# Optimization experiments

Hardware: AMD Instinct MI355X
Metric: run time of the kernel (lower is better)

## Reference

```python
import jax, jax.numpy as jnp
import numpy as np

N = 100000   # nodes
E = 1600000  # edges (avg degree 16)
D = 32       # feature / hidden dim


def setup_inputs() -> dict:
    key = jax.random.key(0)
    k_x, k_e, kq, kk, kv, ko = jax.random.split(key, 6)
    s = 1.0 / np.sqrt(D).astype(np.float32)
    x = jax.random.normal(k_x, (N, D), dtype=jnp.float32)
    edge_index = jax.random.randint(k_e, (2, E), 0, N, dtype=jnp.int64)
    Wq = jax.random.normal(kq, (D, D), dtype=jnp.float32) * s
    Wk = jax.random.normal(kk, (D, D), dtype=jnp.float32) * s
    Wv = jax.random.normal(kv, (D, D), dtype=jnp.float32) * s
    Wo = jax.random.normal(ko, (D, D), dtype=jnp.float32) * s
    return {"x": x, "edge_index": edge_index, "Wq": Wq, "Wk": Wk, "Wv": Wv, "Wo": Wo}


def reference(x, edge_index, Wq, Wk, Wv, Wo):
    sender, receiver = edge_index[0], edge_index[1]
    n = x.shape[0]
    scale = x.shape[1] ** -0.5  # hidden_dim == D
    Q = x @ Wq  # [N, D]
    K = x @ Wk
    V = x @ Wv
    # per-edge attention scores
    scores = jnp.sum(Q[receiver] * K[sender], axis=1) * scale  # [E]
    # numerically-stable segment softmax over incoming edges of each receiver
    smax = jax.ops.segment_max(scores, receiver, num_segments=n)  # [N]
    alpha = jnp.exp(scores - smax[receiver])  # [E]
    Z = jax.ops.segment_sum(alpha, receiver, num_segments=n)  # [N]
    alpha = alpha / (Z[receiver] + 1e-6)
    # weighted aggregation of sender values
    out = jax.ops.segment_sum(alpha[:, None] * V[sender], receiver, num_segments=n)  # [N, D]
    return x + out @ Wo
```

## Files before the change

kernel.cpp:

```cpp
#include <hip/hip_runtime.h>
#include <hip/hip_bf16.h>

#define DIM 32
#define RPB 32
#define RCR 512
#define NCMAX 256
#define CAPC 9216
#define PBLK 256

__device__ __forceinline__ float b2f(ushort h) {
    union { float f; unsigned u; } u; u.u = ((unsigned)h) << 16; return u.f;
}
__device__ __forceinline__ float h2f(ushort u) {
    _Float16 h; __builtin_memcpy(&h, &u, 2); return (float)h;
}
__device__ __forceinline__ ushort f2h(float f) {
    _Float16 h = (_Float16)f; ushort u; __builtin_memcpy(&u, &h, 2); return u;
}

__device__ __forceinline__ int load_idx(const int* __restrict__ idx, size_t pos,
                                        int mode, int n) {
    int v = mode ? idx[2 * pos] : idx[pos];
    return v < 0 ? 0 : (v >= n ? n - 1 : v);
}
__device__ __forceinline__ float load_f(const void* p, size_t i, int bf) {
    return bf ? b2f(((const ushort*)p)[i]) : ((const float*)p)[i];
}

__global__ void __launch_bounds__(256)
qkv_kernel(const void* __restrict__ x_, const void* __restrict__ Wq_,
           const void* __restrict__ Wk_, const void* __restrict__ Wv_,
           int N, int nc, ushort* __restrict__ Q, ushort* __restrict__ KV,
           unsigned* __restrict__ gcur) {
    __shared__ float sW[3][DIM * DIM];
    __shared__ float sx[8][DIM];
    __shared__ int sBf;

    const int tid = threadIdx.x;
    if (tid < 64) {
        int e = (((const ushort*)x_)[2 * tid] >> 7) & 0xFF;
        unsigned long long bb = __ballot(e >= 100 && e <= 135);
        if (tid == 0) sBf = (__popcll(bb) >= 56);
    }
    if (blockIdx.x == 0) {
        for (int i = tid; i < nc; i += 256) gcur[i] = (unsigned)i * CAPC;
    }
    __syncthreads();
    const int bf = sBf;

    for (int i = tid; i < DIM * DIM; i += 256) {
        sW[0][i] = load_f(Wq_, i, bf);
        sW[1][i] = load_f(Wk_, i, bf);
        sW[2][i] = load_f(Wv_, i, bf);
    }
    const int lr  = tid >> 5;
    const int d   = tid & 31;
    const int row = blockIdx.x * 8 + lr;
    if (row < N) sx[lr][d] = load_f(x_, (size_t)row * DIM + d, bf);
    __syncthreads();
    if (row >= N) return;

    float aq = 0.f, ak = 0.f, av = 0.f;
#pragma unroll
    for (int k = 0; k < DIM; ++k) {
        const float xk = sx[lr][k];
        aq += xk * sW[0][k * DIM + d];
        ak += xk * sW[1][k * DIM + d];
        av += xk * sW[2][k * DIM + d];
    }
    Q[(size_t)row * DIM + d]      = f2h(aq * 0.17677669529663687f);
    KV[(size_t)row * 64 + d]      = f2h(ak);
    KV[(size_t)row * 64 + 32 + d] = f2h(av);
}

__global__ void __launch_bounds__(256)
place_kernel(const int* __restrict__ idx, int E, int N, int nc,
             unsigned* __restrict__ gcur, unsigned* __restrict__ bedges) {
    __shared__ int h[NCMAX];
    __shared__ int goff[NCMAX];
    __shared__ int sMode;

    const int tid = threadIdx.x;
    if (tid < 64) {
        unsigned long long mm = __ballot(idx[2 * tid + 1] != 0);
        if (tid == 0) sMode = (mm == 0ULL);
    }
    for (int i = tid; i < nc; i += 256) h[i] = 0;
    __syncthreads();
    const int mode = sMode;

    const int per = (E + gridDim.x - 1) / gridDim.x;
    const int e0 = blockIdx.x * per;
    const int e1 = min(e0 + per, E);

    for (int e = e0 + tid; e < e1; e += 256) {
        const int r = load_idx(idx, (size_t)E + e, mode, N);
        atomicAdd(&h[r >> 9], 1);
    }
    __syncthreads();
    for (int i = tid; i < nc; i += 256) {
        const int v = h[i];
        goff[i] = v ? (int)atomicAdd(&gcur[i], (unsigned)v) : 0;
        h[i] = 0;
    }
    __syncthreads();
    for (int e = e0 + tid; e < e1; e += 256) {
        const int r = load_idx(idx, (size_t)E + e, mode, N);
        const int s = load_idx(idx, (size_t)e, mode, N);
        const int cb = r >> 9;
        const int p = goff[cb] + atomicAdd(&h[cb], 1);
        if (p < (cb + 1) * CAPC)
            bedges[p] = (unsigned)s | ((unsigned)(r & (RCR - 1)) << 17);
    }
}

__global__ void __launch_bounds__(1024)
rsort_kernel(unsigned* __restrict__ bedges, const unsigned* __restrict__ gcur,
             int* __restrict__ rbase, int* __restrict__ rcount) {
    __shared__ unsigned eL[CAPC];
    __shared__ int cnt[RCR];
    __shared__ int wsum[8];

    const int tid = threadIdx.x;
    const int c = blockIdx.x;
    const unsigned s0 = (unsigned)c * CAPC;
    int m = (int)(gcur[c] - s0);
    if (m < 0) m = 0; if (m > CAPC) m = CAPC;

    if (tid < RCR) cnt[tid] = 0;
    __syncthreads();
    for (int i = tid; i < m; i += 1024) {
        const unsigned e = bedges[s0 + i];
        eL[i] = e;
        atomicAdd(&cnt[(e >> 17) & (RCR - 1)], 1);
    }
    __syncthreads();

    const int lane = tid & 63, w = tid >> 6;
    const int v = (tid < RCR) ? cnt[tid] : 0;
    int x = v;
#pragma unroll
    for (int o = 1; o < 64; o <<= 1) { int t = __shfl_up(x, o); if (lane >= o) x += t; }
    if (tid < RCR && lane == 63) wsum[w] = x;
    __syncthreads();
    if (tid == 0) {
        int a = 0;
#pragma unroll
        for (int k = 0; k < 8; ++k) { int t = wsum[k]; wsum[k] = a; a += t; }
    }
    __syncthreads();
    int excl = 0;
    if (tid < RCR) {
        excl = x - v + wsum[w];
        rbase[c * RCR + tid]  = (int)s0 + excl;
        rcount[c * RCR + tid] = v;
    }
    __syncthreads();
    if (tid < RCR) cnt[tid] = (int)s0 + excl;
    __syncthreads();
    for (int i = tid; i < m; i += 1024) {
        const unsigned e = eL[i];
        const int p = atomicAdd(&cnt[(e >> 17) & (RCR - 1)], 1);
        bedges[p] = e & 0x1FFFF;
    }
}

__global__ void __launch_bounds__(256)
agg_kernel(const ushort* __restrict__ Q, const ushort* __restrict__ KV,
           const unsigned* __restrict__ bedges, const int* __restrict__ rbase,
           const int* __restrict__ rcount, const void* __restrict__ x_,
           const void* __restrict__ Wo_, int N, float* __restrict__ out) {
    __shared__ float sWo[DIM * DIM];
    __shared__ float accS[RPB][DIM + 1];
    __shared__ float Zs[RPB];
    __shared__ unsigned sQ[RPB * 16];
    __shared__ int sBf;

    const int tid = threadIdx.x;
    if (tid < 64) {
        int e = (((const ushort*)x_)[2 * tid] >> 7) & 0xFF;
        unsigned long long bb = __ballot(e >= 100 && e <= 135);
        if (tid == 0) sBf = (__popcll(bb) >= 56);
    }
    const int r0 = blockIdx.x * RPB;
    const int nr = min(RPB, N - r0);
    __syncthreads();
    const int bf = sBf;

    for (int i = tid; i < DIM * DIM; i += 256) sWo[i] = load_f(Wo_, i, bf);
    for (int i = tid; i < nr * 16; i += 256)
        sQ[i] = ((const unsigned*)(Q + (size_t)r0 * DIM))[i];
    __syncthreads();

    const int w    = tid >> 6;
    const int lane = tid & 63;
    const int i8   = lane >> 3;
    const int j    = lane & 7;

    for (int rl = w; rl < nr; rl += 4) {
        const int r   = r0 + rl;
        const int deg = rcount[r];
        const int o0  = rbase[r];
        const ushort4 qh = *(const ushort4*)((const ushort*)sQ + rl * DIM + j * 4);
        const float q0 = h2f(qh.x), q1 = h2f(qh.y), q2 = h2f(qh.z), q3 = h2f(qh.w);

        float ax = 0.f, ay = 0.f, az = 0.f, aw = 0.f, zs = 0.f;
        const int chunks = (deg + 7) >> 3;
        const int dm1 = deg - 1;

        int cc = 0;
        for (; cc + 2 <= chunks; cc += 2) {
            const int c0 = cc * 8 + i8;
            const int c1 = c0 + 8;
            const bool ok0 = (c0 < deg);
            const bool ok1 = (c1 < deg);
            const int s0 = (int)bedges[o0 + (ok0 ? c0 : dm1)];
            const int s1 = (int)bedges[o0 + (ok1 ? c1 : dm1)];
            const ushort* kvA = KV + (size_t)s0 * 64;
            const ushort* kvB = KV + (size_t)s1 * 64;

            const ushort4 khA = *(const ushort4*)(kvA + j * 4);
            const ushort4 vhA = *(const ushort4*)(kvA + 32 + j * 4);
            const ushort4 khB = *(const ushort4*)(kvB + j * 4);
            const ushort4 vhB = *(const ushort4*)(kvB + 32 + j * 4);

            float pA = h2f(khA.x) * q0;
            float pB = h2f(khB.x) * q0;
            pA = fmaf(h2f(khA.y), q1, pA);  pB = fmaf(h2f(khB.y), q1, pB);
            pA = fmaf(h2f(khA.z), q2, pA);  pB = fmaf(h2f(khB.z), q2, pB);
            pA = fmaf(h2f(khA.w), q3, pA);  pB = fmaf(h2f(khB.w), q3, pB);

            pA += __shfl_xor(pA, 1);        pB += __shfl_xor(pB, 1);
            pA += __shfl_xor(pA, 2);        pB += __shfl_xor(pB, 2);
            pA += __shfl_xor(pA, 4);        pB += __shfl_xor(pB, 4);

            pA = fminf(fmaxf(pA, -60.f), 60.f);
            pB = fminf(fmaxf(pB, -60.f), 60.f);
            const float aA = ok0 ? __expf(pA) : 0.f;
            const float aB = ok1 ? __expf(pB) : 0.f;

            ax = fmaf(h2f(vhA.x), aA, ax);  ax = fmaf(h2f(vhB.x), aB, ax);
            ay = fmaf(h2f(vhA.y), aA, ay);  ay = fmaf(h2f(vhB.y), aB, ay);
            az = fmaf(h2f(vhA.z), aA, az);  az = fmaf(h2f(vhB.z), aB, az);
            aw = fmaf(h2f(vhA.w), aA, aw);  aw = fmaf(h2f(vhB.w), aB, aw);
            zs += aA + aB;
        }
        if (cc < chunks) {
            const int c = cc * 8 + i8;
            const bool ok = (c < deg);
            const int s = (int)bedges[o0 + (ok ? c : dm1)];
            const ushort* kv = KV + (size_t)s * 64;
            const ushort4 kh = *(const ushort4*)(kv + j * 4);
            const ushort4 vh = *(const ushort4*)(kv + 32 + j * 4);

            float p = h2f(kh.x) * q0;
            p = fmaf(h2f(kh.y), q1, p);
            p = fmaf(h2f(kh.z), q2, p);
            p = fmaf(h2f(kh.w), q3, p);
            p += __shfl_xor(p, 1);
            p += __shfl_xor(p, 2);
            p += __shfl_xor(p, 4);
            p = fminf(fmaxf(p, -60.f), 60.f);
            const float a = ok ? __expf(p) : 0.f;

            ax = fmaf(h2f(vh.x), a, ax);
            ay = fmaf(h2f(vh.y), a, ay);
            az = fmaf(h2f(vh.z), a, az);
            aw = fmaf(h2f(vh.w), a, aw);
            zs += a;
        }
#pragma unroll
        for (int o = 8; o < 64; o <<= 1) {
            ax += __shfl_xor(ax, o); ay += __shfl_xor(ay, o);
            az += __shfl_xor(az, o); aw += __shfl_xor(aw, o);
            zs += __shfl_xor(zs, o);
        }
        if (i8 == 0) {
            float* ar = accS[rl];
            ar[j * 4 + 0] = ax; ar[j * 4 + 1] = ay;
            ar[j * 4 + 2] = az; ar[j * 4 + 3] = aw;
            if (j == 0) Zs[rl] = zs;
        }
    }
    __syncthreads();

    const int lr = tid >> 5;
    const int d  = tid & 31;
#pragma unroll
    for (int it = 0; it < RPB / 8; ++it) {
        const int rl = it * 8 + lr;
        if (rl < nr) {
            const float inv = 1.f / (Zs[rl] + 1e-6f);
            float o = 0.f;
#pragma unroll
            for (int k = 0; k < DIM; ++k) o += accS[rl][k] * sWo[k * DIM + d];
            const size_t oi = (size_t)(r0 + rl) * DIM + d;
            out[oi] = load_f(x_, oi, bf) + inv * o;
        }
    }
}

extern "C" void kernel_launch(void* const* d_in, const int* in_sizes, int n_in,
                              void* d_out, int out_size, void* d_ws, size_t ws_size,
                              hipStream_t stream) {
    const void* x   = d_in[0];
    const int*  idx = (const int*)d_in[1];
    const void* Wq  = d_in[2];
    const void* Wk  = d_in[3];
    const void* Wv  = d_in[4];
    const void* Wo  = d_in[5];
    float* out = (float*)d_out;

    const int N = in_sizes[0] / DIM;
    const int E = in_sizes[1] / 2;
    const int nc = (N + RCR - 1) / RCR;
    const size_t N32 = (size_t)N * DIM;

    ushort*   Q      = (ushort*)d_ws;
    ushort*   KV     = Q + N32;
    unsigned* bedges = (unsigned*)(KV + (size_t)N * 64);
    unsigned* gcur   = bedges + (size_t)nc * CAPC;
    int*      rbase  = (int*)(gcur + NCMAX);
    int*      rcount = rbase + (size_t)nc * RCR;

    qkv_kernel<<<(N + 7) / 8, 256, 0, stream>>>(x, Wq, Wk, Wv, N, nc, Q, KV, gcur);
    place_kernel<<<PBLK, 256, 0, stream>>>(idx, E, N, nc, gcur, bedges);
    rsort_kernel<<<nc, 1024, 0, stream>>>(bedges, gcur, rbase, rcount);
    agg_kernel<<<(N + RPB - 1) / RPB, 256, 0, stream>>>(Q, KV, bedges, rbase,
                                                        rcount, x, Wo, N, out);
}
```

Baseline: 212.3 us.

## Fuse four kernels into one cooperative persistent kernel with grid syncs

Merges the QKV projection, edge bucket placement, per-chunk receiver sort and attention aggregation into a single cooperative kernel with 256 blocks of 1024 threads. Phases are separated by grid.sync(), and shared memory is reused across phases through a union. The aim is to remove the launch gaps between kernels. In exchange, occupancy drops to one large block per CU with a fixed grid, the aggregation phase loses the fine-grained scheduling of many small blocks, and each phase waits on grid-wide barriers.

```diff
diff --git a/kernel.cpp b/kernel.cpp
--- a/kernel.cpp
+++ b/kernel.cpp
@@ -1,12 +1,15 @@
 #include <hip/hip_runtime.h>
 #include <hip/hip_bf16.h>
+#include <hip/hip_cooperative_groups.h>
+
+namespace cg = cooperative_groups;
 
 #define DIM 32
-#define RPB 32
 #define RCR 512
 #define NCMAX 256
 #define CAPC 9216
-#define PBLK 256
+#define GRID 256
+#define BLK 1024
 
 __device__ __forceinline__ float b2f(ushort h) {
     union { float f; unsigned u; } u; u.u = ((unsigned)h) << 16; return u.f;
@@ -17,7 +20,6 @@
 __device__ __forceinline__ ushort f2h(float f) {
     _Float16 h = (_Float16)f; ushort u; __builtin_memcpy(&u, &h, 2); return u;
 }
-
 __device__ __forceinline__ int load_idx(const int* __restrict__ idx, size_t pos,
                                         int mode, int n) {
     int v = mode ? idx[2 * pos] : idx[pos];
@@ -27,275 +29,264 @@
     return bf ? b2f(((const ushort*)p)[i]) : ((const float*)p)[i];
 }
 
-__global__ void __launch_bounds__(256)
-qkv_kernel(const void* __restrict__ x_, const void* __restrict__ Wq_,
-           const void* __restrict__ Wk_, const void* __restrict__ Wv_,
-           int N, int nc, ushort* __restrict__ Q, ushort* __restrict__ KV,
-           unsigned* __restrict__ gcur) {
-    __shared__ float sW[3][DIM * DIM];
-    __shared__ float sx[8][DIM];
-    __shared__ int sBf;
+union SMem {
+    struct { float sW[3][DIM * DIM]; float sx[32][DIM]; } qkv;
+    struct { int h[NCMAX]; int goff[NCMAX]; } place;
+    struct { unsigned eL[CAPC]; int cnt[RCR]; int wsum[16]; } sort;
+    struct { float sWo[DIM * DIM]; unsigned sQ[128 * 16];
+             float accS[128][DIM + 1]; float Zs[128]; } agg;
+};
+
+__global__ void __launch_bounds__(BLK)
+mega_kernel(const void* __restrict__ x_, const int* __restrict__ idx,
+            const void* __restrict__ Wq_, const void* __restrict__ Wk_,
+            const void* __restrict__ Wv_, const void* __restrict__ Wo_,
+            int N, int E, int nc,
+            ushort* __restrict__ Q, ushort* __restrict__ KV,
+            unsigned* __restrict__ bedges, unsigned* __restrict__ gcur,
+            int* __restrict__ rbase, int* __restrict__ rcount,
+            float* __restrict__ out) {
+    cg::grid_group grid = cg::this_grid();
+    __shared__ SMem sm;
+    __shared__ int sBf, sMode;
 
     const int tid = threadIdx.x;
+
     if (tid < 64) {
         int e = (((const ushort*)x_)[2 * tid] >> 7) & 0xFF;
         unsigned long long bb = __ballot(e >= 100 && e <= 135);
-        if (tid == 0) sBf = (__popcll(bb) >= 56);
+        unsigned long long mm = __ballot(idx[2 * tid + 1] != 0);
+        if (tid == 0) { sBf = (__popcll(bb) >= 56); sMode = (mm == 0ULL); }
     }
     if (blockIdx.x == 0) {
-        for (int i = tid; i < nc; i += 256) gcur[i] = (unsigned)i * CAPC;
+        for (int i = tid; i < nc; i += BLK) gcur[i] = (unsigned)i * CAPC;
     }
     __syncthreads();
-    const int bf = sBf;
-
-    for (int i = tid; i < DIM * DIM; i += 256) {
-        sW[0][i] = load_f(Wq_, i, bf);
-        sW[1][i] = load_f(Wk_, i, bf);
-        sW[2][i] = load_f(Wv_, i, bf);
-    }
-    const int lr  = tid >> 5;
-    const int d   = tid & 31;
-    const int row = blockIdx.x * 8 + lr;
-    if (row < N) sx[lr][d] = load_f(x_, (size_t)row * DIM + d, bf);
-    __syncthreads();
-    if (row >= N) return;
-
-    float aq = 0.f, ak = 0.f, av = 0.f;
-#pragma unroll
-    for (int k = 0; k < DIM; ++k) {
-        const float xk = sx[lr][k];
-        aq += xk * sW[0][k * DIM + d];
-        ak += xk * sW[1][k * DIM + d];
-        av += xk * sW[2][k * DIM + d];
-    }
-    Q[(size_t)row * DIM + d]      = f2h(aq * 0.17677669529663687f);
-    KV[(size_t)row * 64 + d]      = f2h(ak);
-    KV[(size_t)row * 64 + 32 + d] = f2h(av);
-}
-
-__global__ void __launch_bounds__(256)
-place_kernel(const int* __restrict__ idx, int E, int N, int nc,
-             unsigned* __restrict__ gcur, unsigned* __restrict__ bedges) {
-    __shared__ int h[NCMAX];
-    __shared__ int goff[NCMAX];
-    __shared__ int sMode;
-
-    const int tid = threadIdx.x;
-    if (tid < 64) {
-        unsigned long long mm = __ballot(idx[2 * tid + 1] != 0);
-        if (tid == 0) sMode = (mm == 0ULL);
-    }
-    for (int i = tid; i < nc; i += 256) h[i] = 0;
-    __syncthreads();
-    const int mode = sMode;
-
-    const int per = (E + gridDim.x - 1) / gridDim.x;
-    const int e0 = blockIdx.x * per;
-    const int e1 = min(e0 + per, E);
-
-    for (int e = e0 + tid; e < e1; e += 256) {
-        const int r = load_idx(idx, (size_t)E + e, mode, N);
-        atomicAdd(&h[r >> 9], 1);
-    }
-    __syncthreads();
-    for (int i = tid; i < nc; i += 256) {
-        const int v = h[i];
-        goff[i] = v ? (int)atomicAdd(&gcur[i], (unsigned)v) : 0;
-        h[i] = 0;
-    }
-    __syncthreads();
-    for (int e = e0 + tid; e < e1; e += 256) {
-        const int r = load_idx(idx, (size_t)E + e, mode, N);
-        const int s = load_idx(idx, (size_t)e, mode, N);
-        const int cb = r >> 9;
-        const int p = goff[cb] + atomicAdd(&h[cb], 1);
-        if (p < (cb + 1) * CAPC)
-            bedges[p] = (unsigned)s | ((unsigned)(r & (RCR - 1)) << 17);
-    }
-}
-
-__global__ void __launch_bounds__(1024)
-rsort_kernel(unsigned* __restrict__ bedges, const unsigned* __restrict__ gcur,
-             int* __restrict__ rbase, int* __restrict__ rcount) {
-    __shared__ unsigned eL[CAPC];
-    __shared__ int cnt[RCR];
-    __shared__ int wsum[8];
-
-    const int tid = threadIdx.x;
-    const int c = blockIdx.x;
-    const unsigned s0 = (unsigned)c * CAPC;
-    int m = (int)(gcur[c] - s0);
-    if (m < 0) m = 0; if (m > CAPC) m = CAPC;
-
-    if (tid < RCR) cnt[tid] = 0;
-    __syncthreads();
-    for (int i = tid; i < m; i += 1024) {
-        const unsigned e = bedges[s0 + i];
-        eL[i] = e;
-        atomicAdd(&cnt[(e >> 17) & (RCR - 1)], 1);
-    }
-    __syncthreads();
-
-    const int lane = tid & 63, w = tid >> 6;
-    const int v = (tid < RCR) ? cnt[tid] : 0;
-    int x = v;
-#pragma unroll
-    for (int o = 1; o < 64; o <<= 1) { int t = __shfl_up(x, o); if (lane >= o) x += t; }
-    if (tid < RCR && lane == 63) wsum[w] = x;
-    __syncthreads();
-    if (tid == 0) {
-        int a = 0;
-#pragma unroll
-        for (int k = 0; k < 8; ++k) { int t = wsum[k]; wsum[k] = a; a += t; }
-    }
-    __syncthreads();
-    int excl = 0;
-    if (tid < RCR) {
-        excl = x - v + wsum[w];
-        rbase[c * RCR + tid]  = (int)s0 + excl;
-        rcount[c * RCR + tid] = v;
-    }
-    __syncthreads();
-    if (tid < RCR) cnt[tid] = (int)s0 + excl;
-    __syncthreads();
-    for (int i = tid; i < m; i += 1024) {
-        const unsigned e = eL[i];
-        const int p = atomicAdd(&cnt[(e >> 17) & (RCR - 1)], 1);
-        bedges[p] = e & 0x1FFFF;
-    }
-}
-
-__global__ void __launch_bounds__(256)
-agg_kernel(const ushort* __restrict__ Q, const ushort* __restrict__ KV,
-           const unsigned* __restrict__ bedges, const int* __restrict__ rbase,
-           const int* __restrict__ rcount, const void* __restrict__ x_,
-           const void* __restrict__ Wo_, int N, float* __restrict__ out) {
-    __shared__ float sWo[DIM * DIM];
-    __shared__ float accS[RPB][DIM + 1];
-    __shared__ float Zs[RPB];
-    __shared__ unsigned sQ[RPB * 16];
-    __shared__ int sBf;
-
-    const int tid = threadIdx.x;
-    if (tid < 64) {
-        int e = (((const ushort*)x_)[2 * tid] >> 7) & 0xFF;
-        unsigned long long bb = __ballot(e >= 100 && e <= 135);
-        if (tid == 0) sBf = (__popcll(bb) >= 56);
-    }
-    const int r0 = blockIdx.x * RPB;
-    const int nr = min(RPB, N - r0);
-    __syncthreads();
-    const int bf = sBf;
-
-    for (int i = tid; i < DIM * DIM; i += 256) sWo[i] = load_f(Wo_, i, bf);
-    for (int i = tid; i < nr * 16; i += 256)
-        sQ[i] = ((const unsigned*)(Q + (size_t)r0 * DIM))[i];
-    __syncthreads();
-
-    const int w    = tid >> 6;
-    const int lane = tid & 63;
-    const int i8   = lane >> 3;
-    const int j    = lane & 7;
-
-    for (int rl = w; rl < nr; rl += 4) {
-        const int r   = r0 + rl;
-        const int deg = rcount[r];
-        const int o0  = rbase[r];
-        const ushort4 qh = *(const ushort4*)((const ushort*)sQ + rl * DIM + j * 4);
-        const float q0 = h2f(qh.x), q1 = h2f(qh.y), q2 = h2f(qh.z), q3 = h2f(qh.w);
-
-        float ax = 0.f, ay = 0.f, az = 0.f, aw = 0.f, zs = 0.f;
-        const int chunks = (deg + 7) >> 3;
-        const int dm1 = deg - 1;
-
-        int cc = 0;
-        for (; cc + 2 <= chunks; cc += 2) {
-            const int c0 = cc * 8 + i8;
-            const int c1 = c0 + 8;
-            const bool ok0 = (c0 < deg);
-            const bool ok1 = (c1 < deg);
-            const int s0 = (int)bedges[o0 + (ok0 ? c0 : dm1)];
-            const int s1 = (int)bedges[o0 + (ok1 ? c1 : dm1)];
-            const ushort* kvA = KV + (size_t)s0 * 64;
-            const ushort* kvB = KV + (size_t)s1 * 64;
-
-            const ushort4 khA = *(const ushort4*)(kvA + j * 4);
-            const ushort4 vhA = *(const ushort4*)(kvA + 32 + j * 4);
-            const ushort4 khB = *(const ushort4*)(kvB + j * 4);
-            const ushort4 vhB = *(const ushort4*)(kvB + 32 + j * 4);
-
-            float pA = h2f(khA.x) * q0;
-            float pB = h2f(khB.x) * q0;
-            pA = fmaf(h2f(khA.y), q1, pA);  pB = fmaf(h2f(khB.y), q1, pB);
-            pA = fmaf(h2f(khA.z), q2, pA);  pB = fmaf(h2f(khB.z), q2, pB);
-            pA = fmaf(h2f(khA.w), q3, pA);  pB = fmaf(h2f(khB.w), q3, pB);
-
-            pA += __shfl_xor(pA, 1);        pB += __shfl_xor(pB, 1);
-            pA += __shfl_xor(pA, 2);        pB += __shfl_xor(pB, 2);
-            pA += __shfl_xor(pA, 4);        pB += __shfl_xor(pB, 4);
-
-            pA = fminf(fmaxf(pA, -60.f), 60.f);
-            pB = fminf(fmaxf(pB, -60.f), 60.f);
-            const float aA = ok0 ? __expf(pA) : 0.f;
-            const float aB = ok1 ? __expf(pB) : 0.f;
-
-            ax = fmaf(h2f(vhA.x), aA, ax);  ax = fmaf(h2f(vhB.x), aB, ax);
-            ay = fmaf(h2f(vhA.y), aA, ay);  ay = fmaf(h2f(vhB.y), aB, ay);
-            az = fmaf(h2f(vhA.z), aA, az);  az = fmaf(h2f(vhB.z), aB, az);
-            aw = fmaf(h2f(vhA.w), aA, aw);  aw = fmaf(h2f(vhB.w), aB, aw);
-            zs += aA + aB;
-        }
-        if (cc < chunks) {
-            const int c = cc * 8 + i8;
-            const bool ok = (c < deg);
-            const int s = (int)bedges[o0 + (ok ? c : dm1)];
-            const ushort* kv = KV + (size_t)s * 64;
-            const ushort4 kh = *(const ushort4*)(kv + j * 4);
-            const ushort4 vh = *(const ushort4*)(kv + 32 + j * 4);
-
-            float p = h2f(kh.x) * q0;
-            p = fmaf(h2f(kh.y), q1, p);
-            p = fmaf(h2f(kh.z), q2, p);
-            p = fmaf(h2f(kh.w), q3, p);
-            p += __shfl_xor(p, 1);
-            p += __shfl_xor(p, 2);
-            p += __shfl_xor(p, 4);
-            p = fminf(fmaxf(p, -60.f), 60.f);
-            const float a = ok ? __expf(p) : 0.f;
-
-            ax = fmaf(h2f(vh.x), a, ax);
-            ay = fmaf(h2f(vh.y), a, ay);
-            az = fmaf(h2f(vh.z), a, az);
-            aw = fmaf(h2f(vh.w), a, aw);
-            zs += a;
-        }
-#pragma unroll
-        for (int o = 8; o < 64; o <<= 1) {
-            ax += __shfl_xor(ax, o); ay += __shfl_xor(ay, o);
-            az += __shfl_xor(az, o); aw += __shfl_xor(aw, o);
-            zs += __shfl_xor(zs, o);
-        }
-        if (i8 == 0) {
-            float* ar = accS[rl];
-            ar[j * 4 + 0] = ax; ar[j * 4 + 1] = ay;
-            ar[j * 4 + 2] = az; ar[j * 4 + 3] = aw;
-            if (j == 0) Zs[rl] = zs;
-        }
-    }
-    __syncthreads();
-
-    const int lr = tid >> 5;
-    const int d  = tid & 31;
-#pragma unroll
-    for (int it = 0; it < RPB / 8; ++it) {
-        const int rl = it * 8 + lr;
-        if (rl < nr) {
-            const float inv = 1.f / (Zs[rl] + 1e-6f);
-            float o = 0.f;
-#pragma unroll
-            for (int k = 0; k < DIM; ++k) o += accS[rl][k] * sWo[k * DIM + d];
-            const size_t oi = (size_t)(r0 + rl) * DIM + d;
-            out[oi] = load_f(x_, oi, bf) + inv * o;
+    const int bf = sBf, mode = sMode;
+
+    for (int i = tid; i < DIM * DIM; i += BLK) {
+        sm.qkv.sW[0][i] = load_f(Wq_, i, bf);
+        sm.qkv.sW[1][i] = load_f(Wk_, i, bf);
+        sm.qkv.sW[2][i] = load_f(Wv_, i, bf);
+    }
+    {
+        const int lr = tid >> 5;
+        const int d  = tid & 31;
+        for (int base = blockIdx.x * 32; base < N; base += GRID * 32) {
+            const int row = base + lr;
+            __syncthreads();
+            if (row < N) sm.qkv.sx[lr][d] = load_f(x_, (size_t)row * DIM + d, bf);
+            __syncthreads();
+            if (row < N) {
+                float aq = 0.f, ak = 0.f, av = 0.f;
+#pragma unroll
+                for (int k = 0; k < DIM; ++k) {
+                    const float xk = sm.qkv.sx[lr][k];
+                    aq += xk * sm.qkv.sW[0][k * DIM + d];
+                    ak += xk * sm.qkv.sW[1][k * DIM + d];
+                    av += xk * sm.qkv.sW[2][k * DIM + d];
+                }
+                Q[(size_t)row * DIM + d]      = f2h(aq * 0.17677669529663687f);
+                KV[(size_t)row * 64 + d]      = f2h(ak);
+                KV[(size_t)row * 64 + 32 + d] = f2h(av);
+            }
+        }
+    }
+    grid.sync();
+
+    {
+        const int per = (E + GRID - 1) / GRID;
+        const int e0 = blockIdx.x * per;
+        const int e1 = min(e0 + per, E);
+        for (int i = tid; i < nc; i += BLK) sm.place.h[i] = 0;
+        __syncthreads();
+        for (int e = e0 + tid; e < e1; e += BLK) {
+            const int r = load_idx(idx, (size_t)E + e, mode, N);
+            atomicAdd(&sm.place.h[r >> 9], 1);
+        }
+        __syncthreads();
+        for (int i = tid; i < nc; i += BLK) {
+            const int v = sm.place.h[i];
+            sm.place.goff[i] = v ? (int)atomicAdd(&gcur[i], (unsigned)v) : 0;
+            sm.place.h[i] = 0;
+        }
+        __syncthreads();
+        for (int e = e0 + tid; e < e1; e += BLK) {
+            const int r = load_idx(idx, (size_t)E + e, mode, N);
+            const int s = load_idx(idx, (size_t)e, mode, N);
+            const int cb = r >> 9;
+            const int p = sm.place.goff[cb] + atomicAdd(&sm.place.h[cb], 1);
+            if (p < (cb + 1) * CAPC)
+                bedges[p] = (unsigned)s | ((unsigned)(r & (RCR - 1)) << 17);
+        }
+    }
+    grid.sync();
+
+    for (int c = blockIdx.x; c < nc; c += GRID) {
+        const unsigned s0 = (unsigned)c * CAPC;
+        int m = (int)(gcur[c] - s0);
+        if (m < 0) m = 0; if (m > CAPC) m = CAPC;
+
+        if (tid < RCR) sm.sort.cnt[tid] = 0;
+        __syncthreads();
+        for (int i = tid; i < m; i += BLK) {
+            const unsigned e = bedges[s0 + i];
+            sm.sort.eL[i] = e;
+            atomicAdd(&sm.sort.cnt[(e >> 17) & (RCR - 1)], 1);
+        }
+        __syncthreads();
+
+        const int lane = tid & 63, w = tid >> 6;
+        const int v = (tid < RCR) ? sm.sort.cnt[tid] : 0;
+        int x = v;
+#pragma unroll
+        for (int o = 1; o < 64; o <<= 1) {
+            int t = __shfl_up(x, o); if (lane >= o) x += t;
+        }
+        if (tid < RCR && lane == 63) sm.sort.wsum[w] = x;
+        __syncthreads();
+        if (tid == 0) {
+            int a = 0;
+#pragma unroll
+            for (int k = 0; k < 8; ++k) { int t = sm.sort.wsum[k]; sm.sort.wsum[k] = a; a += t; }
+        }
+        __syncthreads();
+        int excl = 0;
+        if (tid < RCR) {
+            excl = x - v + sm.sort.wsum[w];
+            rbase[c * RCR + tid]  = (int)s0 + excl;
+            rcount[c * RCR + tid] = v;
+        }
+        __syncthreads();
+        if (tid < RCR) sm.sort.cnt[tid] = (int)s0 + excl;
+        __syncthreads();
+        for (int i = tid; i < m; i += BLK) {
+            const unsigned e = sm.sort.eL[i];
+            const int p = atomicAdd(&sm.sort.cnt[(e >> 17) & (RCR - 1)], 1);
+            bedges[p] = e & 0x1FFFF;
+        }
+        __syncthreads();
+    }
+    grid.sync();
+
+    for (int i = tid; i < DIM * DIM; i += BLK) sm.agg.sWo[i] = load_f(Wo_, i, bf);
+    {
+        const int ngrp = (N + 127) >> 7;
+        const int w    = tid >> 6;
+        const int lane = tid & 63;
+        const int i8   = lane >> 3;
+        const int j    = lane & 7;
+        const int lr   = tid >> 5;
+        const int d    = tid & 31;
+
+        for (int g = blockIdx.x; g < ngrp; g += GRID) {
+            const int r0 = g << 7;
+            const int nr = min(128, N - r0);
+            __syncthreads();
+            for (int i = tid; i < nr * 16; i += BLK)
+                sm.agg.sQ[i] = ((const unsigned*)(Q + (size_t)r0 * DIM))[i];
+            __syncthreads();
+
+            for (int rl = w; rl < nr; rl += 16) {
+                const int r   = r0 + rl;
+                const int deg = rcount[r];
+                const int o0  = rbase[r];
+                const ushort4 qh = *(const ushort4*)((const ushort*)sm.agg.sQ + rl * DIM + j * 4);
+                const float q0 = h2f(qh.x), q1 = h2f(qh.y), q2 = h2f(qh.z), q3 = h2f(qh.w);
+
+                float ax = 0.f, ay = 0.f, az = 0.f, aw = 0.f, zs = 0.f;
+                const int chunks = (deg + 7) >> 3;
+                const int dm1 = deg - 1;
+
+                int cc = 0;
+                for (; cc + 2 <= chunks; cc += 2) {
+                    const int c0 = cc * 8 + i8;
+                    const int c1 = c0 + 8;
+                    const bool ok0 = (c0 < deg);
+                    const bool ok1 = (c1 < deg);
+                    const int sA = (int)bedges[o0 + (ok0 ? c0 : dm1)];
+                    const int sB = (int)bedges[o0 + (ok1 ? c1 : dm1)];
+                    const ushort* kvA = KV + (size_t)sA * 64;
+                    const ushort* kvB = KV + (size_t)sB * 64;
+
+                    const ushort4 khA = *(const ushort4*)(kvA + j * 4);
+                    const ushort4 vhA = *(const ushort4*)(kvA + 32 + j * 4);
+                    const ushort4 khB = *(const ushort4*)(kvB + j * 4);
+                    const ushort4 vhB = *(const ushort4*)(kvB + 32 + j * 4);
+
+                    float pA = h2f(khA.x) * q0;
+                    float pB = h2f(khB.x) * q0;
+                    pA = fmaf(h2f(khA.y), q1, pA);  pB = fmaf(h2f(khB.y), q1, pB);
+                    pA = fmaf(h2f(khA.z), q2, pA);  pB = fmaf(h2f(khB.z), q2, pB);
+                    pA = fmaf(h2f(khA.w), q3, pA);  pB = fmaf(h2f(khB.w), q3, pB);
+
+                    pA += __shfl_xor(pA, 1);        pB += __shfl_xor(pB, 1);
+                    pA += __shfl_xor(pA, 2);        pB += __shfl_xor(pB, 2);
+                    pA += __shfl_xor(pA, 4);        pB += __shfl_xor(pB, 4);
+
+                    pA = fminf(fmaxf(pA, -60.f), 60.f);
+                    pB = fminf(fmaxf(pB, -60.f), 60.f);
+                    const float aA = ok0 ? __expf(pA) : 0.f;
+                    const float aB = ok1 ? __expf(pB) : 0.f;
+
+                    ax = fmaf(h2f(vhA.x), aA, ax);  ax = fmaf(h2f(vhB.x), aB, ax);
+                    ay = fmaf(h2f(vhA.y), aA, ay);  ay = fmaf(h2f(vhB.y), aB, ay);
+                    az = fmaf(h2f(vhA.z), aA, az);  az = fmaf(h2f(vhB.z), aB, az);
+                    aw = fmaf(h2f(vhA.w), aA, aw);  aw = fmaf(h2f(vhB.w), aB, aw);
+                    zs += aA + aB;
+                }
+                if (cc < chunks) {
+                    const int c = cc * 8 + i8;
+                    const bool ok = (c < deg);
+                    const int s = (int)bedges[o0 + (ok ? c : dm1)];
+                    const ushort* kv = KV + (size_t)s * 64;
+                    const ushort4 kh = *(const ushort4*)(kv + j * 4);
+                    const ushort4 vh = *(const ushort4*)(kv + 32 + j * 4);
+
+                    float p = h2f(kh.x) * q0;
+                    p = fmaf(h2f(kh.y), q1, p);
+                    p = fmaf(h2f(kh.z), q2, p);
+                    p = fmaf(h2f(kh.w), q3, p);
+                    p += __shfl_xor(p, 1);
+                    p += __shfl_xor(p, 2);
+                    p += __shfl_xor(p, 4);
+                    p = fminf(fmaxf(p, -60.f), 60.f);
+                    const float a = ok ? __expf(p) : 0.f;
+
+                    ax = fmaf(h2f(vh.x), a, ax);
+                    ay = fmaf(h2f(vh.y), a, ay);
+                    az = fmaf(h2f(vh.z), a, az);
+                    aw = fmaf(h2f(vh.w), a, aw);
+                    zs += a;
+                }
+#pragma unroll
+                for (int o = 8; o < 64; o <<= 1) {
+                    ax += __shfl_xor(ax, o); ay += __shfl_xor(ay, o);
+                    az += __shfl_xor(az, o); aw += __shfl_xor(aw, o);
+                    zs += __shfl_xor(zs, o);
+                }
+                if (i8 == 0) {
+                    float* ar = sm.agg.accS[rl];
+                    ar[j * 4 + 0] = ax; ar[j * 4 + 1] = ay;
+                    ar[j * 4 + 2] = az; ar[j * 4 + 3] = aw;
+                    if (j == 0) sm.agg.Zs[rl] = zs;
+                }
+            }
+            __syncthreads();
+
+#pragma unroll
+            for (int it = 0; it < 4; ++it) {
+                const int rl = it * 32 + lr;
+                if (rl < nr) {
+                    const float inv = 1.f / (sm.agg.Zs[rl] + 1e-6f);
+                    float o = 0.f;
+#pragma unroll
+                    for (int k = 0; k < DIM; ++k)
+                        o += sm.agg.accS[rl][k] * sm.agg.sWo[k * DIM + d];
+                    const size_t oi = (size_t)(r0 + rl) * DIM + d;
+                    out[oi] = load_f(x_, oi, bf) + inv * o;
+                }
+            }
         }
     }
 }
@@ -311,9 +302,9 @@
     const void* Wo  = d_in[5];
     float* out = (float*)d_out;
 
-    const int N = in_sizes[0] / DIM;
-    const int E = in_sizes[1] / 2;
-    const int nc = (N + RCR - 1) / RCR;
+    int N = in_sizes[0] / DIM;
+    int E = in_sizes[1] / 2;
+    int nc = (N + RCR - 1) / RCR;
     const size_t N32 = (size_t)N * DIM;
 
     ushort*   Q      = (ushort*)d_ws;
@@ -323,9 +314,10 @@
     int*      rbase  = (int*)(gcur + NCMAX);
     int*      rcount = rbase + (size_t)nc * RCR;
 
-    qkv_kernel<<<(N + 7) / 8, 256, 0, stream>>>(x, Wq, Wk, Wv, N, nc, Q, KV, gcur);
-    place_kernel<<<PBLK, 256, 0, stream>>>(idx, E, N, nc, gcur, bedges);
-    rsort_kernel<<<nc, 1024, 0, stream>>>(bedges, gcur, rbase, rcount);
-    agg_kernel<<<(N + RPB - 1) / RPB, 256, 0, stream>>>(Q, KV, bedges, rbase,
-                                                        rcount, x, Wo, N, out);
-}
+    void* args[] = { (void*)&x, (void*)&idx, (void*)&Wq, (void*)&Wk,
+                     (void*)&Wv, (void*)&Wo, (void*)&N, (void*)&E, (void*)&nc,
+                     (void*)&Q, (void*)&KV, (void*)&bedges, (void*)&gcur,
+                     (void*)&rbase, (void*)&rcount, (void*)&out };
+    hipLaunchCooperativeKernel((const void*)mega_kernel, dim3(GRID), dim3(BLK),
+                               args, 0, stream);
+}
```

Result: slower. 335.1 us (+57.8%).

## Fuse edge placement with QKV and sorting with aggregation into two kernels

Applied to the files above, without the earlier changes.

Cuts the four-kernel pipeline down to two. The edge-bucketing pass now runs in extra blocks of the QKV projection kernel. Each placement block writes into fixed per-chunk sub-regions padded with sentinels, which removes the global counters and the histogram pre-pass. The per-receiver counting sort moves into the aggregation kernel, where each block scans its chunk's region, keeps only its quarter of receivers, and sorts them into shared memory. This saves launches and global round-trips for the sorted edge list. In exchange, each chunk region is scanned by four blocks, and the fixed sub-capacities can silently drop edges on skewed degree distributions.

```diff
diff --git a/kernel.cpp b/kernel.cpp
--- a/kernel.cpp
+++ b/kernel.cpp
@@ -2,11 +2,13 @@
 #include <hip/hip_bf16.h>
 
 #define DIM 32
-#define RPB 32
 #define RCR 512
 #define NCMAX 256
-#define CAPC 9216
-#define PBLK 256
+#define PBLK 64
+#define SUBCAP 200
+#define REGSZ (PBLK * SUBCAP)
+#define QCAP 2432
+#define SENT 0xFFFFFFFFu
 
 __device__ __forceinline__ float b2f(ushort h) {
     union { float f; unsigned u; } u; u.u = ((unsigned)h) << 16; return u.f;
@@ -17,7 +19,6 @@
 __device__ __forceinline__ ushort f2h(float f) {
     _Float16 h = (_Float16)f; ushort u; __builtin_memcpy(&u, &h, 2); return u;
 }
-
 __device__ __forceinline__ int load_idx(const int* __restrict__ idx, size_t pos,
                                         int mode, int n) {
     int v = mode ? idx[2 * pos] : idx[pos];
@@ -27,13 +28,92 @@
     return bf ? b2f(((const ushort*)p)[i]) : ((const float*)p)[i];
 }
 
+union K1Smem {
+    struct { float sW[3][DIM * DIM]; float sx[8][DIM]; } qkv;
+    struct { int h[NCMAX]; } place;
+};
+
 __global__ void __launch_bounds__(256)
-qkv_kernel(const void* __restrict__ x_, const void* __restrict__ Wq_,
-           const void* __restrict__ Wk_, const void* __restrict__ Wv_,
-           int N, int nc, ushort* __restrict__ Q, ushort* __restrict__ KV,
-           unsigned* __restrict__ gcur) {
-    __shared__ float sW[3][DIM * DIM];
-    __shared__ float sx[8][DIM];
+qkv_place_kernel(const void* __restrict__ x_, const int* __restrict__ idx,
+                 const void* __restrict__ Wq_, const void* __restrict__ Wk_,
+                 const void* __restrict__ Wv_, int N, int E, int nc,
+                 ushort* __restrict__ Q, ushort* __restrict__ KV,
+                 unsigned* __restrict__ bedges) {
+    __shared__ K1Smem sm;
+    __shared__ int sBf, sMode;
+
+    const int tid = threadIdx.x;
+    if (tid < 64) {
+        int e = (((const ushort*)x_)[2 * tid] >> 7) & 0xFF;
+        unsigned long long bb = __ballot(e >= 100 && e <= 135);
+        unsigned long long mm = __ballot(idx[2 * tid + 1] != 0);
+        if (tid == 0) { sBf = (__popcll(bb) >= 56); sMode = (mm == 0ULL); }
+    }
+    __syncthreads();
+    const int bf = sBf, mode = sMode;
+
+    if (blockIdx.x < PBLK) {
+        const int pb = blockIdx.x;
+        for (int i = tid; i < nc; i += 256) sm.place.h[i] = 0;
+        __syncthreads();
+        const int per = (E + PBLK - 1) / PBLK;
+        const int e0 = pb * per;
+        const int e1 = min(e0 + per, E);
+        for (int e = e0 + tid; e < e1; e += 256) {
+            const int r = load_idx(idx, (size_t)E + e, mode, N);
+            const int s = load_idx(idx, (size_t)e, mode, N);
+            const int cb = r >> 9;
+            const int p = atomicAdd(&sm.place.h[cb], 1);
+            if (p < SUBCAP)
+                bedges[(size_t)cb * REGSZ + pb * SUBCAP + p] =
+                    (unsigned)s | ((unsigned)(r & (RCR - 1)) << 17);
+        }
+        __syncthreads();
+        for (int i = tid; i < nc * SUBCAP; i += 256) {
+            const int c = i / SUBCAP;
+            const int q = i - c * SUBCAP;
+            if (q >= sm.place.h[c])
+                bedges[(size_t)c * REGSZ + pb * SUBCAP + q] = SENT;
+        }
+        return;
+    }
+
+    for (int i = tid; i < DIM * DIM; i += 256) {
+        sm.qkv.sW[0][i] = load_f(Wq_, i, bf);
+        sm.qkv.sW[1][i] = load_f(Wk_, i, bf);
+        sm.qkv.sW[2][i] = load_f(Wv_, i, bf);
+    }
+    const int lr  = tid >> 5;
+    const int d   = tid & 31;
+    const int row = (blockIdx.x - PBLK) * 8 + lr;
+    if (row < N) sm.qkv.sx[lr][d] = load_f(x_, (size_t)row * DIM + d, bf);
+    __syncthreads();
+    if (row >= N) return;
+
+    float aq = 0.f, ak = 0.f, av = 0.f;
+#pragma unroll
+    for (int k = 0; k < DIM; ++k) {
+        const float xk = sm.qkv.sx[lr][k];
+        aq += xk * sm.qkv.sW[0][k * DIM + d];
+        ak += xk * sm.qkv.sW[1][k * DIM + d];
+        av += xk * sm.qkv.sW[2][k * DIM + d];
+    }
+    Q[(size_t)row * DIM + d]      = f2h(aq * 0.17677669529663687f);
+    KV[(size_t)row * 64 + d]      = f2h(ak);
+    KV[(size_t)row * 64 + 32 + d] = f2h(av);
+}
+
+__global__ void __launch_bounds__(256)
+sortagg_kernel(const ushort* __restrict__ Q, const ushort* __restrict__ KV,
+               const unsigned* __restrict__ bedges, const void* __restrict__ x_,
+               const void* __restrict__ Wo_, int N, float* __restrict__ out) {
+    __shared__ unsigned eS[QCAP];
+    __shared__ int h[128], off[128], cur[128];
+    __shared__ int wsum[2];
+    __shared__ unsigned sQ[128 * 16];
+    __shared__ float accS[128][DIM + 1];
+    __shared__ float Zs[128];
+    __shared__ float sWo[DIM * DIM];
     __shared__ int sBf;
 
     const int tid = threadIdx.x;
@@ -42,154 +122,50 @@
         unsigned long long bb = __ballot(e >= 100 && e <= 135);
         if (tid == 0) sBf = (__popcll(bb) >= 56);
     }
-    if (blockIdx.x == 0) {
-        for (int i = tid; i < nc; i += 256) gcur[i] = (unsigned)i * CAPC;
-    }
+    const int c  = blockIdx.x >> 2;
+    const int qd = blockIdx.x & 3;
+    const int r0 = c * RCR + qd * 128;
+    const int nr = min(128, N - r0);
+    if (tid < 128) h[tid] = 0;
     __syncthreads();
     const int bf = sBf;
-
-    for (int i = tid; i < DIM * DIM; i += 256) {
-        sW[0][i] = load_f(Wq_, i, bf);
-        sW[1][i] = load_f(Wk_, i, bf);
-        sW[2][i] = load_f(Wv_, i, bf);
-    }
-    const int lr  = tid >> 5;
-    const int d   = tid & 31;
-    const int row = blockIdx.x * 8 + lr;
-    if (row < N) sx[lr][d] = load_f(x_, (size_t)row * DIM + d, bf);
-    __syncthreads();
-    if (row >= N) return;
-
-    float aq = 0.f, ak = 0.f, av = 0.f;
-#pragma unroll
-    for (int k = 0; k < DIM; ++k) {
-        const float xk = sx[lr][k];
-        aq += xk * sW[0][k * DIM + d];
-        ak += xk * sW[1][k * DIM + d];
-        av += xk * sW[2][k * DIM + d];
-    }
-    Q[(size_t)row * DIM + d]      = f2h(aq * 0.17677669529663687f);
-    KV[(size_t)row * 64 + d]      = f2h(ak);
-    KV[(size_t)row * 64 + 32 + d] = f2h(av);
-}
-
-__global__ void __launch_bounds__(256)
-place_kernel(const int* __restrict__ idx, int E, int N, int nc,
-             unsigned* __restrict__ gcur, unsigned* __restrict__ bedges) {
-    __shared__ int h[NCMAX];
-    __shared__ int goff[NCMAX];
-    __shared__ int sMode;
-
-    const int tid = threadIdx.x;
-    if (tid < 64) {
-        unsigned long long mm = __ballot(idx[2 * tid + 1] != 0);
-        if (tid == 0) sMode = (mm == 0ULL);
-    }
-    for (int i = tid; i < nc; i += 256) h[i] = 0;
-    __syncthreads();
-    const int mode = sMode;
-
-    const int per = (E + gridDim.x - 1) / gridDim.x;
-    const int e0 = blockIdx.x * per;
-    const int e1 = min(e0 + per, E);
-
-    for (int e = e0 + tid; e < e1; e += 256) {
-        const int r = load_idx(idx, (size_t)E + e, mode, N);
-        atomicAdd(&h[r >> 9], 1);
-    }
-    __syncthreads();
-    for (int i = tid; i < nc; i += 256) {
-        const int v = h[i];
-        goff[i] = v ? (int)atomicAdd(&gcur[i], (unsigned)v) : 0;
-        h[i] = 0;
-    }
-    __syncthreads();
-    for (int e = e0 + tid; e < e1; e += 256) {
-        const int r = load_idx(idx, (size_t)E + e, mode, N);
-        const int s = load_idx(idx, (size_t)e, mode, N);
-        const int cb = r >> 9;
-        const int p = goff[cb] + atomicAdd(&h[cb], 1);
-        if (p < (cb + 1) * CAPC)
-            bedges[p] = (unsigned)s | ((unsigned)(r & (RCR - 1)) << 17);
-    }
-}
-
-__global__ void __launch_bounds__(1024)
-rsort_kernel(unsigned* __restrict__ bedges, const unsigned* __restrict__ gcur,
-             int* __restrict__ rbase, int* __restrict__ rcount) {
-    __shared__ unsigned eL[CAPC];
-    __shared__ int cnt[RCR];
-    __shared__ int wsum[8];
-
-    const int tid = threadIdx.x;
-    const int c = blockIdx.x;
-    const unsigned s0 = (unsigned)c * CAPC;
-    int m = (int)(gcur[c] - s0);
-    if (m < 0) m = 0; if (m > CAPC) m = CAPC;
-
-    if (tid < RCR) cnt[tid] = 0;
-    __syncthreads();
-    for (int i = tid; i < m; i += 1024) {
-        const unsigned e = bedges[s0 + i];
-        eL[i] = e;
-        atomicAdd(&cnt[(e >> 17) & (RCR - 1)], 1);
-    }
-    __syncthreads();
-
-    const int lane = tid & 63, w = tid >> 6;
-    const int v = (tid < RCR) ? cnt[tid] : 0;
-    int x = v;
-#pragma unroll
-    for (int o = 1; o < 64; o <<= 1) { int t = __shfl_up(x, o); if (lane >= o) x += t; }
-    if (tid < RCR && lane == 63) wsum[w] = x;
-    __syncthreads();
-    if (tid == 0) {
-        int a = 0;
-#pragma unroll
-        for (int k = 0; k < 8; ++k) { int t = wsum[k]; wsum[k] = a; a += t; }
-    }
-    __syncthreads();
-    int excl = 0;
-    if (tid < RCR) {
-        excl = x - v + wsum[w];
-        rbase[c * RCR + tid]  = (int)s0 + excl;
-        rcount[c * RCR + tid] = v;
-    }
-    __syncthreads();
-    if (tid < RCR) cnt[tid] = (int)s0 + excl;
-    __syncthreads();
-    for (int i = tid; i < m; i += 1024) {
-        const unsigned e = eL[i];
-        const int p = atomicAdd(&cnt[(e >> 17) & (RCR - 1)], 1);
-        bedges[p] = e & 0x1FFFF;
-    }
-}
-
-__global__ void __launch_bounds__(256)
-agg_kernel(const ushort* __restrict__ Q, const ushort* __restrict__ KV,
-           const unsigned* __restrict__ bedges, const int* __restrict__ rbase,
-           const int* __restrict__ rcount, const void* __restrict__ x_,
-           const void* __restrict__ Wo_, int N, float* __restrict__ out) {
-    __shared__ float sWo[DIM * DIM];
-    __shared__ float accS[RPB][DIM + 1];
-    __shared__ float Zs[RPB];
-    __shared__ unsigned sQ[RPB * 16];
-    __shared__ int sBf;
-
-    const int tid = threadIdx.x;
-    if (tid < 64) {
-        int e = (((const ushort*)x_)[2 * tid] >> 7) & 0xFF;
-        unsigned long long bb = __ballot(e >= 100 && e <= 135);
-        if (tid == 0) sBf = (__popcll(bb) >= 56);
-    }
-    const int r0 = blockIdx.x * RPB;
-    const int nr = min(RPB, N - r0);
-    __syncthreads();
-    const int bf = sBf;
+    if (nr <= 0) return;
 
     for (int i = tid; i < DIM * DIM; i += 256) sWo[i] = load_f(Wo_, i, bf);
     for (int i = tid; i < nr * 16; i += 256)
         sQ[i] = ((const unsigned*)(Q + (size_t)r0 * DIM))[i];
+
+    const unsigned* reg = bedges + (size_t)c * REGSZ;
+    for (int i = tid; i < REGSZ; i += 256) {
+        const unsigned e = reg[i];
+        if (e != SENT && (int)((e >> 24) & 3) == qd)
+            atomicAdd(&h[(e >> 17) & 127], 1);
+    }
+    __syncthreads();
+    {
+        const int lane = tid & 63, w2 = tid >> 6;
+        const int v = (tid < 128) ? h[tid] : 0;
+        int x = v;
+#pragma unroll
+        for (int o = 1; o < 64; o <<= 1) {
+            int t = __shfl_up(x, o); if (lane >= o) x += t;
+        }
+        if (tid < 128 && lane == 63) wsum[w2] = x;
+        __syncthreads();
+        if (tid < 128) {
+            const int base = (w2 == 1) ? wsum[0] : 0;
+            off[tid] = base + x - v;
+            cur[tid] = off[tid];
+        }
+    }
+    __syncthreads();
+    for (int i = tid; i < REGSZ; i += 256) {
+        const unsigned e = reg[i];
+        if (e != SENT && (int)((e >> 24) & 3) == qd) {
+            const int p = atomicAdd(&cur[(e >> 17) & 127], 1);
+            if (p < QCAP) eS[p] = e & 0x1FFFF;
+        }
+    }
     __syncthreads();
 
     const int w    = tid >> 6;
@@ -198,9 +174,8 @@
     const int j    = lane & 7;
 
     for (int rl = w; rl < nr; rl += 4) {
-        const int r   = r0 + rl;
-        const int deg = rcount[r];
-        const int o0  = rbase[r];
+        const int deg = h[rl];
+        const int o0  = off[rl];
         const ushort4 qh = *(const ushort4*)((const ushort*)sQ + rl * DIM + j * 4);
         const float q0 = h2f(qh.x), q1 = h2f(qh.y), q2 = h2f(qh.z), q3 = h2f(qh.w);
 
@@ -214,10 +189,10 @@
             const int c1 = c0 + 8;
             const bool ok0 = (c0 < deg);
             const bool ok1 = (c1 < deg);
-            const int s0 = (int)bedges[o0 + (ok0 ? c0 : dm1)];
-            const int s1 = (int)bedges[o0 + (ok1 ? c1 : dm1)];
-            const ushort* kvA = KV + (size_t)s0 * 64;
-            const ushort* kvB = KV + (size_t)s1 * 64;
+            const int sA = (int)eS[o0 + (ok0 ? c0 : dm1)];
+            const int sB = (int)eS[o0 + (ok1 ? c1 : dm1)];
+            const ushort* kvA = KV + (size_t)sA * 64;
+            const ushort* kvB = KV + (size_t)sB * 64;
 
             const ushort4 khA = *(const ushort4*)(kvA + j * 4);
             const ushort4 vhA = *(const ushort4*)(kvA + 32 + j * 4);
@@ -246,9 +221,9 @@
             zs += aA + aB;
         }
         if (cc < chunks) {
-            const int c = cc * 8 + i8;
-            const bool ok = (c < deg);
-            const int s = (int)bedges[o0 + (ok ? c : dm1)];
+            const int cx = cc * 8 + i8;
+            const bool ok = (cx < deg);
+            const int s = (int)eS[o0 + (ok ? cx : dm1)];
             const ushort* kv = KV + (size_t)s * 64;
             const ushort4 kh = *(const ushort4*)(kv + j * 4);
             const ushort4 vh = *(const ushort4*)(kv + 32 + j * 4);
@@ -286,8 +261,8 @@
 
     const int lr = tid >> 5;
     const int d  = tid & 31;
-#pragma unroll
-    for (int it = 0; it < RPB / 8; ++it) {
+#pragma unroll 4
+    for (int it = 0; it < 16; ++it) {
         const int rl = it * 8 + lr;
         if (rl < nr) {
             const float inv = 1.f / (Zs[rl] + 1e-6f);
@@ -319,13 +294,10 @@
     ushort*   Q      = (ushort*)d_ws;
     ushort*   KV     = Q + N32;
     unsigned* bedges = (unsigned*)(KV + (size_t)N * 64);
-    unsigned* gcur   = bedges + (size_t)nc * CAPC;
-    int*      rbase  = (int*)(gcur + NCMAX);
-    int*      rcount = rbase + (size_t)nc * RCR;
-
-    qkv_kernel<<<(N + 7) / 8, 256, 0, stream>>>(x, Wq, Wk, Wv, N, nc, Q, KV, gcur);
-    place_kernel<<<PBLK, 256, 0, stream>>>(idx, E, N, nc, gcur, bedges);
-    rsort_kernel<<<nc, 1024, 0, stream>>>(bedges, gcur, rbase, rcount);
-    agg_kernel<<<(N + RPB - 1) / RPB, 256, 0, stream>>>(Q, KV, bedges, rbase,
-                                                        rcount, x, Wo, N, out);
-}
+
+    const int qkv_blocks = (N + 7) / 8;
+    qkv_place_kernel<<<PBLK + qkv_blocks, 256, 0, stream>>>(
+        x, idx, Wq, Wk, Wv, N, E, nc, Q, KV, bedges);
+
+    sortagg_kernel<<<nc * 4, 256, 0, stream>>>(Q, KV, bedges, x, Wo, N, out);
+}
```

New measurement: 310.7 us. 1.46x slower.
